# Kernel optimization log

Hardware: AMD Instinct MI355X
Metric: run time of the kernel (lower is better)

Reference implementation:

```python
import jax, jax.numpy as jnp
import numpy as np

N_NODES = 100000
N_EDGES = 3200000
N_SG = 800000  # edges in the softmax-normalized segment
RULES = 9

SUB_MAT = np.array([[-0.2, -0.1, -0.05, -0.05, -0.05, -0.01, -0.055, -0.01, 0.0],
                    [0.0, -0.002, -0.001, -0.001, -0.001, -0.0002, 0.0008, -0.0002, 0.0]], dtype=np.float32)
SUB_BIAS = np.array([1, 0.7, 0.275, 0.4, 0.25, 0.07, 0.2225, 0.07, 0], dtype=np.float32)


def setup_inputs() -> dict:
    key = jax.random.key(0)
    k1, k2, k3 = jax.random.split(key, 3)
    feat = jax.random.normal(k1, (N_NODES, 4), dtype=jnp.float32)
    src = jax.random.randint(k2, (N_EDGES,), 0, N_NODES)
    dst = jax.random.randint(k3, (N_EDGES,), 0, N_NODES)
    edge_sg_ID = jnp.arange(N_SG, dtype=jnp.int64 if jax.config.read('jax_enable_x64') else jnp.int32).reshape(1, N_SG)
    return {
        'feat': feat,
        'src': src,
        'dst': dst,
        'edge_sg_ID': edge_sg_ID,
        'sub_systems_mat': jnp.asarray(SUB_MAT),
        'sub_systems_bias': jnp.asarray(SUB_BIAS),
    }


def _gauss(x, mean, sigma):
    return jnp.exp(-(x - mean) ** 2 / (2.0 * sigma ** 2))


def _ante_generator(vector):
    # vector: [E, 4] = (dpos_x, dpos_y, dvel_x, dvel_y)
    d = vector[:, :2]
    v = vector[:, 2:]
    x1 = jnp.linalg.norm(d, axis=1, keepdims=True)  # distance, [E,1]
    vnorm = jnp.linalg.norm(v, axis=1, keepdims=True)
    cos = jnp.sum(d * v, axis=1, keepdims=True) / (x1 * vnorm + 1e-8)
    x2 = jnp.degrees(jnp.arccos(jnp.clip(cos, -1.0 + 1e-6, 1.0 - 1e-6)))  # angle deg, [E,1]
    return x1, x2


def _ante_process(x1, x2):
    # memberships: x1 small/med/large, x2 small/med/large
    m1 = [_gauss(x1, 0.0, 0.75), _gauss(x1, 2.0, 0.75), _gauss(x1, 4.0, 0.75)]
    m2 = [_gauss(x2, 0.0, 30.0), _gauss(x2, 90.0, 30.0), _gauss(x2, 180.0, 30.0)]
    # 9 rules: min over all (x1_level, x2_level) pairs -> [E, 1, 9]
    return jnp.stack([jnp.minimum(a, b) for a in m1 for b in m2], axis=2)


def _forward(feat, sub_systems_mat, sub_systems_bias, src, dst, edge_sg_ID):
    vector = feat[dst] - feat[src]  # [E, 4]
    x1, x2 = _ante_generator(vector)  # each [E, 1]
    truth = _ante_process(x1, x2)  # [E, 1, 9]
    premises = jnp.stack((x1, x2), axis=2).reshape(-1, 2)  # [E, 2]
    consequence = premises @ sub_systems_mat + sub_systems_bias  # [E, 9]
    consequence = consequence.reshape(x1.shape[0], x1.shape[1], RULES)  # [E, 1, 9]
    attention = jnp.sum(truth * consequence, axis=2) / jnp.sum(truth, axis=2)  # [E, 1]
    attention = attention[:, :, None]  # [E, 1, 1]
    idx = edge_sg_ID[0]
    # segment softmax over the selected edges (dim 0)
    attention = attention.at[idx].set(jax.nn.softmax(attention[idx], axis=0))
    return attention


def reference(feat, src, dst, edge_sg_ID, sub_systems_mat, sub_systems_bias):
    return _forward(feat, sub_systems_mat, sub_systems_bias, src, dst, edge_sg_ID)
```

## Files before the change

### kernel.cpp

```cpp
#include <hip/hip_runtime.h>


#define N_EDGES 3200000
#define N_SG    800000
#define RULES   9
#define BLOCK   256
#define TOT_GROUPS (N_EDGES / 4)
#define SG_GROUPS  (N_SG / 4)
#define NTHREADS   (TOT_GROUPS / 2)
#define GRID1      ((NTHREADS + BLOCK - 1) / BLOCK)
#define SOFT_T     (SG_GROUPS / 2)
#define NSOFTBLK   ((SOFT_T + BLOCK - 1) / BLOCK)
#define GRID2      ((SG_GROUPS + BLOCK - 1) / BLOCK)

typedef float vf4 __attribute__((ext_vector_type(4)));
typedef int   vi4 __attribute__((ext_vector_type(4)));

__device__ __forceinline__ float fast_acos_deg(float x)
{
    float ax = fabsf(x);
    float p = fmaf(ax, -0.0187293f, 0.0742610f);
    p = fmaf(p, ax, -0.2121144f);
    p = fmaf(p, ax, 1.5707288f);
    float r = __builtin_amdgcn_sqrtf(1.0f - ax) * p;
    r = (x < 0.0f) ? (3.14159265358979f - r) : r;
    return r * 57.29577951308232f;
}

__device__ __forceinline__ float edge_attn(vf4 fd, vf4 fs,
                                           const float* c1, const float* c2,
                                           const float* cb)
{
    float d0 = fd.x - fs.x, d1 = fd.y - fs.y;
    float v0 = fd.z - fs.z, v1 = fd.w - fs.w;

    float d2  = fmaf(d0, d0, d1 * d1);
    float v2  = fmaf(v0, v0, v1 * v1);
    float x1  = __builtin_amdgcn_sqrtf(d2);
    float dot = fmaf(d0, v0, d1 * v1);
    float cosv = dot * __builtin_amdgcn_rcpf(
                     __builtin_amdgcn_sqrtf(d2 * v2) + 1e-8f);
    cosv = fminf(fmaxf(cosv, -1.0f + 1e-6f), 1.0f - 1e-6f);
    float x2 = fast_acos_deg(cosv);

    const float k1 = 0.888888888888889f;
    const float k2 = 5.555555555555556e-4f;
    float m1[3], m2[3];
    float a;
    a = x1;          m1[0] = __expf(-a * a * k1);
    a = x1 - 2.0f;   m1[1] = __expf(-a * a * k1);
    a = x1 - 4.0f;   m1[2] = __expf(-a * a * k1);
    a = x2;          m2[0] = __expf(-a * a * k2);
    a = x2 - 90.0f;  m2[1] = __expf(-a * a * k2);
    a = x2 - 180.0f; m2[2] = __expf(-a * a * k2);

    float num = 0.0f, den = 0.0f;
#pragma unroll
    for (int i = 0; i < 3; ++i) {
#pragma unroll
        for (int j = 0; j < 3; ++j) {
            int r = i * 3 + j;
            float t = fminf(m1[i], m2[j]);
            float c = fmaf(x1, c1[r], fmaf(x2, c2[r], cb[r]));
            num = fmaf(t, c, num);
            den += t;
        }
    }
    return num * __builtin_amdgcn_rcpf(den);
}

__global__ __launch_bounds__(BLOCK, 6) void edge_kernel(
    const vf4*   __restrict__ feat,
    const vi4*   __restrict__ src4,
    const vi4*   __restrict__ dst4,
    const float* __restrict__ M,
    const float* __restrict__ B,
    vf4*         __restrict__ out4,
    float*       __restrict__ partials)
{
    const int t = blockIdx.x * BLOCK + threadIdx.x;

    float c1[RULES], c2[RULES], cb[RULES];
#pragma unroll
    for (int r = 0; r < RULES; ++r) {
        c1[r] = M[r];
        c2[r] = M[RULES + r];
        cb[r] = B[r];
    }

    float s = 0.0f;
    if (t < NTHREADS) {
        const int g0 = 2 * t, g1 = 2 * t + 1;

        vi4 s0 = src4[g0];
        vi4 d0 = dst4[g0];
        vi4 s1 = src4[g1];
        vi4 d1 = dst4[g1];

        vf4 a0 = feat[s0.x], a1 = feat[s0.y], a2 = feat[s0.z], a3 = feat[s0.w];
        vf4 b0 = feat[d0.x], b1 = feat[d0.y], b2 = feat[d0.z], b3 = feat[d0.w];
        vf4 e0 = feat[s1.x], e1 = feat[s1.y], e2 = feat[s1.z], e3 = feat[s1.w];
        vf4 f0 = feat[d1.x], f1 = feat[d1.y], f2 = feat[d1.z], f3 = feat[d1.w];

        vf4 ra, rb;
        ra.x = edge_attn(b0, a0, c1, c2, cb);
        ra.y = edge_attn(b1, a1, c1, c2, cb);
        ra.z = edge_attn(b2, a2, c1, c2, cb);
        ra.w = edge_attn(b3, a3, c1, c2, cb);
        rb.x = edge_attn(f0, e0, c1, c2, cb);
        rb.y = edge_attn(f1, e1, c1, c2, cb);
        rb.z = edge_attn(f2, e2, c1, c2, cb);
        rb.w = edge_attn(f3, e3, c1, c2, cb);

        const bool soft = (t < SOFT_T);
        if (soft) {
            ra.x = __expf(ra.x); ra.y = __expf(ra.y);
            ra.z = __expf(ra.z); ra.w = __expf(ra.w);
            rb.x = __expf(rb.x); rb.y = __expf(rb.y);
            rb.z = __expf(rb.z); rb.w = __expf(rb.w);
            s = ((ra.x + ra.y) + (ra.z + ra.w))
              + ((rb.x + rb.y) + (rb.z + rb.w));
            out4[g0] = ra;
            out4[g1] = rb;
        } else {
            __builtin_nontemporal_store(ra, &out4[g0]);
            __builtin_nontemporal_store(rb, &out4[g1]);
        }
    }

    if (blockIdx.x < NSOFTBLK) {
#pragma unroll
        for (int o = 32; o > 0; o >>= 1) s += __shfl_down(s, o, 64);
        __shared__ float wsum[BLOCK / 64];
        if ((threadIdx.x & 63) == 0) wsum[threadIdx.x >> 6] = s;
        __syncthreads();
        if (threadIdx.x == 0)
            partials[blockIdx.x] = wsum[0] + wsum[1] + wsum[2] + wsum[3];
    }
}

__global__ __launch_bounds__(BLOCK, 8) void scale_kernel(
    const float* __restrict__ partials,
    vf4*         __restrict__ out4)
{
    float s = 0.0f;
    for (int p = threadIdx.x; p < NSOFTBLK; p += BLOCK) s += partials[p];
#pragma unroll
    for (int o = 32; o > 0; o >>= 1) s += __shfl_down(s, o, 64);

    __shared__ float wsum[BLOCK / 64];
    __shared__ float stot;
    if ((threadIdx.x & 63) == 0) wsum[threadIdx.x >> 6] = s;
    __syncthreads();
    if (threadIdx.x == 0) stot = wsum[0] + wsum[1] + wsum[2] + wsum[3];
    __syncthreads();

    const float inv = 1.0f / stot;
    const int i = blockIdx.x * BLOCK + threadIdx.x;
    if (i < SG_GROUPS) {
        vf4 v = out4[i];
        v.x *= inv; v.y *= inv; v.z *= inv; v.w *= inv;
        __builtin_nontemporal_store(v, &out4[i]);
    }
}

extern "C" void kernel_launch(void* const* d_in, const int* in_sizes, int n_in,
                              void* d_out, int out_size, void* d_ws, size_t ws_size,
                              hipStream_t stream)
{
    const vf4*   feat = (const vf4*)d_in[0];
    const vi4*   src4 = (const vi4*)d_in[1];
    const vi4*   dst4 = (const vi4*)d_in[2];
    const float* M    = (const float*)d_in[4];
    const float* B    = (const float*)d_in[5];
    vf4*   out4     = (vf4*)d_out;
    float* partials = (float*)d_ws;

    edge_kernel<<<dim3(GRID1), dim3(BLOCK), 0, stream>>>(
        feat, src4, dst4, M, B, out4, partials);
    scale_kernel<<<dim3(GRID2), dim3(BLOCK), 0, stream>>>(partials, out4);
}
```

Measured before the change: 117.1 us.

## Fuse softmax normalization into edge kernel via grid-wide counter barrier

```diff
diff --git a/kernel.cpp b/kernel.cpp
--- a/kernel.cpp
+++ b/kernel.cpp
@@ -11,7 +11,10 @@
 #define GRID1      ((NTHREADS + BLOCK - 1) / BLOCK)
 #define SOFT_T     (SG_GROUPS / 2)
 #define NSOFTBLK   ((SOFT_T + BLOCK - 1) / BLOCK)
-#define GRID2      ((SG_GROUPS + BLOCK - 1) / BLOCK)
+#define DONE_CNT   (NSOFTBLK + 1)
+
+#define WS_TOTAL_IDX   396
+#define WS_COUNTER_IDX 400
 
 typedef float vf4 __attribute__((ext_vector_type(4)));
 typedef int   vi4 __attribute__((ext_vector_type(4)));
@@ -69,16 +72,27 @@
     return num * __builtin_amdgcn_rcpf(den);
 }
 
-__global__ __launch_bounds__(BLOCK, 6) void edge_kernel(
+__global__ __launch_bounds__(64) void init_kernel(float* __restrict__ ws)
+{
+    if (threadIdx.x == 0)
+        __hip_atomic_store((int*)(ws + WS_COUNTER_IDX), 0,
+                           __ATOMIC_RELAXED, __HIP_MEMORY_SCOPE_AGENT);
+}
+
+__global__ __launch_bounds__(BLOCK, 4) void edge_kernel(
     const vf4*   __restrict__ feat,
     const vi4*   __restrict__ src4,
     const vi4*   __restrict__ dst4,
     const float* __restrict__ M,
     const float* __restrict__ B,
     vf4*         __restrict__ out4,
-    float*       __restrict__ partials)
+    float*       __restrict__ ws)
 {
     const int t = blockIdx.x * BLOCK + threadIdx.x;
+
+    __shared__ float wsum[BLOCK / 64];
+    __shared__ float stot_sh;
+    __shared__ int   last_sh;
 
     float c1[RULES], c2[RULES], cb[RULES];
 #pragma unroll
@@ -89,8 +103,12 @@
     }
 
     float s = 0.0f;
+    vf4 ra, rb;
+    int g0 = 0, g1 = 0;
+    bool soft = false;
+
     if (t < NTHREADS) {
-        const int g0 = 2 * t, g1 = 2 * t + 1;
+        g0 = 2 * t; g1 = 2 * t + 1;
 
         vi4 s0 = src4[g0];
         vi4 d0 = dst4[g0];
@@ -102,7 +120,6 @@
         vf4 e0 = feat[s1.x], e1 = feat[s1.y], e2 = feat[s1.z], e3 = feat[s1.w];
         vf4 f0 = feat[d1.x], f1 = feat[d1.y], f2 = feat[d1.z], f3 = feat[d1.w];
 
-        vf4 ra, rb;
         ra.x = edge_attn(b0, a0, c1, c2, cb);
         ra.y = edge_attn(b1, a1, c1, c2, cb);
         ra.z = edge_attn(b2, a2, c1, c2, cb);
@@ -112,7 +129,7 @@
         rb.z = edge_attn(f2, e2, c1, c2, cb);
         rb.w = edge_attn(f3, e3, c1, c2, cb);
 
-        const bool soft = (t < SOFT_T);
+        soft = (t < SOFT_T);
         if (soft) {
             ra.x = __expf(ra.x); ra.y = __expf(ra.y);
             ra.z = __expf(ra.z); ra.w = __expf(ra.w);
@@ -120,8 +137,6 @@
             rb.z = __expf(rb.z); rb.w = __expf(rb.w);
             s = ((ra.x + ra.y) + (ra.z + ra.w))
               + ((rb.x + rb.y) + (rb.z + rb.w));
-            out4[g0] = ra;
-            out4[g1] = rb;
         } else {
             __builtin_nontemporal_store(ra, &out4[g0]);
             __builtin_nontemporal_store(rb, &out4[g1]);
@@ -129,38 +144,61 @@
     }
 
     if (blockIdx.x < NSOFTBLK) {
+        float*   partials = ws;
+        float*   total    = ws + WS_TOTAL_IDX;
+        int*     counter  = (int*)(ws + WS_COUNTER_IDX);
+
 #pragma unroll
         for (int o = 32; o > 0; o >>= 1) s += __shfl_down(s, o, 64);
-        __shared__ float wsum[BLOCK / 64];
         if ((threadIdx.x & 63) == 0) wsum[threadIdx.x >> 6] = s;
         __syncthreads();
-        if (threadIdx.x == 0)
-            partials[blockIdx.x] = wsum[0] + wsum[1] + wsum[2] + wsum[3];
-    }
-}
-
-__global__ __launch_bounds__(BLOCK, 8) void scale_kernel(
-    const float* __restrict__ partials,
-    vf4*         __restrict__ out4)
-{
-    float s = 0.0f;
-    for (int p = threadIdx.x; p < NSOFTBLK; p += BLOCK) s += partials[p];
-#pragma unroll
-    for (int o = 32; o > 0; o >>= 1) s += __shfl_down(s, o, 64);
-
-    __shared__ float wsum[BLOCK / 64];
-    __shared__ float stot;
-    if ((threadIdx.x & 63) == 0) wsum[threadIdx.x >> 6] = s;
-    __syncthreads();
-    if (threadIdx.x == 0) stot = wsum[0] + wsum[1] + wsum[2] + wsum[3];
-    __syncthreads();
-
-    const float inv = 1.0f / stot;
-    const int i = blockIdx.x * BLOCK + threadIdx.x;
-    if (i < SG_GROUPS) {
-        vf4 v = out4[i];
-        v.x *= inv; v.y *= inv; v.z *= inv; v.w *= inv;
-        __builtin_nontemporal_store(v, &out4[i]);
+        if (threadIdx.x == 0) {
+            float ps = wsum[0] + wsum[1] + wsum[2] + wsum[3];
+            __hip_atomic_store(&partials[blockIdx.x], ps,
+                               __ATOMIC_RELAXED, __HIP_MEMORY_SCOPE_AGENT);
+            int old = __hip_atomic_fetch_add(counter, 1,
+                               __ATOMIC_ACQ_REL, __HIP_MEMORY_SCOPE_AGENT);
+            last_sh = (old == NSOFTBLK - 1);
+        }
+        __syncthreads();
+
+        if (last_sh) {
+            float ts = 0.0f;
+            if (threadIdx.x < NSOFTBLK)
+                ts = __hip_atomic_load(&partials[threadIdx.x],
+                          __ATOMIC_RELAXED, __HIP_MEMORY_SCOPE_AGENT);
+            if (threadIdx.x + 256 < NSOFTBLK)
+                ts += __hip_atomic_load(&partials[threadIdx.x + 256],
+                          __ATOMIC_RELAXED, __HIP_MEMORY_SCOPE_AGENT);
+#pragma unroll
+            for (int o = 32; o > 0; o >>= 1) ts += __shfl_down(ts, o, 64);
+            if ((threadIdx.x & 63) == 0) wsum[threadIdx.x >> 6] = ts;
+            __syncthreads();
+            if (threadIdx.x == 0) {
+                float tot = wsum[0] + wsum[1] + wsum[2] + wsum[3];
+                __hip_atomic_store(total, tot,
+                                   __ATOMIC_RELAXED, __HIP_MEMORY_SCOPE_AGENT);
+                __hip_atomic_fetch_add(counter, 1,
+                                   __ATOMIC_RELEASE, __HIP_MEMORY_SCOPE_AGENT);
+            }
+        }
+
+        if (threadIdx.x == 0) {
+            while (__hip_atomic_load(counter, __ATOMIC_ACQUIRE,
+                                     __HIP_MEMORY_SCOPE_AGENT) != DONE_CNT)
+                __builtin_amdgcn_s_sleep(2);
+            stot_sh = __hip_atomic_load(total, __ATOMIC_RELAXED,
+                                        __HIP_MEMORY_SCOPE_AGENT);
+        }
+        __syncthreads();
+
+        if (soft) {
+            float inv = 1.0f / stot_sh;
+            ra *= inv;
+            rb *= inv;
+            __builtin_nontemporal_store(ra, &out4[g0]);
+            __builtin_nontemporal_store(rb, &out4[g1]);
+        }
     }
 }
 
@@ -173,10 +211,10 @@
     const vi4*   dst4 = (const vi4*)d_in[2];
     const float* M    = (const float*)d_in[4];
     const float* B    = (const float*)d_in[5];
-    vf4*   out4     = (vf4*)d_out;
-    float* partials = (float*)d_ws;
-
+    vf4*   out4 = (vf4*)d_out;
+    float* ws   = (float*)d_ws;
+
+    init_kernel<<<dim3(1), dim3(64), 0, stream>>>(ws);
     edge_kernel<<<dim3(GRID1), dim3(BLOCK), 0, stream>>>(
-        feat, src4, dst4, M, B, out4, partials);
-    scale_kernel<<<dim3(GRID2), dim3(BLOCK), 0, stream>>>(partials, out4);
-}
+        feat, src4, dst4, M, B, out4, ws);
+}
```

New measurement: 153.1 us. +30.8%, slower.
